# Performance work log

Hardware: AMD Instinct MI355X
Metric: run time of the kernel (lower is better)

Reference implementation:

```python
import jax, jax.numpy as jnp
import numpy as np

N = 100000
E = 1600000
D_IN = 128
D_OUT = 128
BN_EPS = 1e-5


def setup_inputs() -> dict:
    key = jax.random.key(0)
    k1, k2, k3, k4 = jax.random.split(key, 4)
    x = jax.random.normal(k1, (N, D_IN), dtype=jnp.float32)
    edge_index = jax.random.randint(k2, (2, E), 0, N, dtype=jnp.int64)
    # Linear params (torch: y = x @ W.T + b)
    lim = 1.0 / np.sqrt(D_IN)
    W = jax.random.uniform(k3, (D_OUT, D_IN), minval=-lim, maxval=lim, dtype=jnp.float32)
    b = jax.random.uniform(k4, (D_OUT,), minval=-lim, maxval=lim, dtype=jnp.float32)
    # BatchNorm1d affine params (torch defaults: weight=1, bias=0)
    gamma = jnp.ones((D_OUT,), dtype=jnp.float32)
    beta = jnp.zeros((D_OUT,), dtype=jnp.float32)
    return {"x": x, "edge_index": edge_index, "W": W, "b": b,
            "gamma": gamma, "beta": beta, "batch_size": 32}


def reference(x, edge_index, W, b, gamma, beta, batch_size):
    # Linear
    h = x @ W.T + b  # (N, D_OUT)
    num_nodes = h.shape[0]
    row, col = edge_index[0], edge_index[1]
    # Gather neighbor features and scatter-add into destination rows
    agg = jax.ops.segment_sum(h[col], row, num_segments=num_nodes)  # (N, D_OUT)
    cnt = jax.ops.segment_sum(jnp.ones((edge_index.shape[1], 1), dtype=h.dtype),
                              row, num_segments=num_nodes)  # (N, 1)
    agg = agg / (cnt + 1e-8)
    # Residual
    h = h + agg
    # BatchNorm1d, training mode (batch statistics, biased variance)
    mean = jnp.mean(h, axis=0)
    var = jnp.mean((h - mean) ** 2, axis=0)
    out = (h - mean) * jax.lax.rsqrt(var + BN_EPS) * gamma + beta
    return out
```

## Files before the change

kernel.cpp:

```cpp
#include <hip/hip_runtime.h>

#define BN_EPS_F 1e-5f
#define MAXB 128
#define BIN_CHUNK 4096
#define BIN_EPT 16

static __device__ __forceinline__ float bf2f(unsigned short u) {
  union { unsigned int i; float f; } c; c.i = ((unsigned int)u) << 16; return c.f;
}
static __device__ __forceinline__ unsigned short f2bf(float f) {
  union { float f; unsigned int i; } c; c.f = f;
  unsigned int r = c.i + 0x7FFFu + ((c.i >> 16) & 1u);
  return (unsigned short)(r >> 16);
}

__global__ void transpose_W_kernel(const float* __restrict__ W, float* __restrict__ Wt) {
  int idx = blockIdx.x * 256 + threadIdx.x;
  if (idx < 128 * 128) {
    int j = idx >> 7, k = idx & 127;
    Wt[(k << 7) + j] = W[idx];
  }
}

__global__ __launch_bounds__(256) void linear_kernel(
    const float* __restrict__ x, const float* __restrict__ Wt,
    const float* __restrict__ bias, unsigned short* __restrict__ h, int n_nodes) {
  __shared__ float xt[32 * 128];
  const int t = threadIdx.x;
  const int tile = blockIdx.x << 5;
  {
    const float4* xg = reinterpret_cast<const float4*>(x) + ((size_t)tile << 5);
    float4* xl = reinterpret_cast<float4*>(xt);
#pragma unroll
    for (int i = 0; i < 4; ++i) xl[t + i * 256] = xg[t + i * 256];
  }
  __syncthreads();
  const int jq = (t & 31) << 2;
  const int g = t >> 5;
  const float* xr0 = &xt[(g * 4 + 0) << 7];
  const float* xr1 = &xt[(g * 4 + 1) << 7];
  const float* xr2 = &xt[(g * 4 + 2) << 7];
  const float* xr3 = &xt[(g * 4 + 3) << 7];
  float4 a0 = {0, 0, 0, 0}, a1 = {0, 0, 0, 0}, a2 = {0, 0, 0, 0}, a3 = {0, 0, 0, 0};
#pragma unroll 8
  for (int k = 0; k < 128; ++k) {
    float4 w = *reinterpret_cast<const float4*>(&Wt[(k << 7) + jq]);
    float x0 = xr0[k], x1 = xr1[k], x2 = xr2[k], x3 = xr3[k];
    a0.x = fmaf(x0, w.x, a0.x); a0.y = fmaf(x0, w.y, a0.y);
    a0.z = fmaf(x0, w.z, a0.z); a0.w = fmaf(x0, w.w, a0.w);
    a1.x = fmaf(x1, w.x, a1.x); a1.y = fmaf(x1, w.y, a1.y);
    a1.z = fmaf(x1, w.z, a1.z); a1.w = fmaf(x1, w.w, a1.w);
    a2.x = fmaf(x2, w.x, a2.x); a2.y = fmaf(x2, w.y, a2.y);
    a2.z = fmaf(x2, w.z, a2.z); a2.w = fmaf(x2, w.w, a2.w);
    a3.x = fmaf(x3, w.x, a3.x); a3.y = fmaf(x3, w.y, a3.y);
    a3.z = fmaf(x3, w.z, a3.z); a3.w = fmaf(x3, w.w, a3.w);
  }
  float4 bb = *reinterpret_cast<const float4*>(&bias[jq]);
  a0.x += bb.x; a0.y += bb.y; a0.z += bb.z; a0.w += bb.w;
  a1.x += bb.x; a1.y += bb.y; a1.z += bb.z; a1.w += bb.w;
  a2.x += bb.x; a2.y += bb.y; a2.z += bb.z; a2.w += bb.w;
  a3.x += bb.x; a3.y += bb.y; a3.z += bb.z; a3.w += bb.w;
  const int nb = tile + (g << 2);
  ushort4 p0 = {f2bf(a0.x), f2bf(a0.y), f2bf(a0.z), f2bf(a0.w)};
  ushort4 p1 = {f2bf(a1.x), f2bf(a1.y), f2bf(a1.z), f2bf(a1.w)};
  ushort4 p2 = {f2bf(a2.x), f2bf(a2.y), f2bf(a2.z), f2bf(a2.w)};
  ushort4 p3 = {f2bf(a3.x), f2bf(a3.y), f2bf(a3.z), f2bf(a3.w)};
  *reinterpret_cast<ushort4*>(&h[((size_t)(nb + 0) << 7) + jq]) = p0;
  *reinterpret_cast<ushort4*>(&h[((size_t)(nb + 1) << 7) + jq]) = p1;
  *reinterpret_cast<ushort4*>(&h[((size_t)(nb + 2) << 7) + jq]) = p2;
  *reinterpret_cast<ushort4*>(&h[((size_t)(nb + 3) << 7) + jq]) = p3;
}

__global__ __launch_bounds__(256) void bucket_hist_kernel(
    const int* __restrict__ row, int* __restrict__ bhist, int e_total, int nb) {
  __shared__ int bh[MAXB];
  const int t = threadIdx.x;
  if (t < MAXB) bh[t] = 0;
  __syncthreads();
  int i = blockIdx.x * 256 + t;
  const int stride = gridDim.x * 256;
  for (; i < e_total; i += stride) atomicAdd(&bh[row[i] >> 10], 1);
  __syncthreads();
  if (t < nb) {
    int c = bh[t];
    if (c) atomicAdd(&bhist[t], c);
  }
}

__global__ void bucket_scan_kernel(const int* __restrict__ bhist, int* __restrict__ bbase,
                                   int* __restrict__ bcursor, int nb, int e_total) {
  __shared__ int sd[MAXB];
  const int t = threadIdx.x;
  int v = (t < nb) ? bhist[t] : 0;
  sd[t] = v;
  __syncthreads();
  for (int off = 1; off < MAXB; off <<= 1) {
    int u = (t >= off) ? sd[t - off] : 0;
    __syncthreads();
    sd[t] += u;
    __syncthreads();
  }
  int excl = sd[t] - v;
  if (t < nb) { bbase[t] = excl; bcursor[t] = excl; }
  if (t == 0) bbase[nb] = e_total;
}

__global__ __launch_bounds__(256) void bin_kernel(
    const int* __restrict__ row, const int* __restrict__ col,
    int* __restrict__ bcursor, unsigned int* __restrict__ pairs, int e_total, int nb) {
  __shared__ int scount[MAXB];
  __shared__ int gbase[MAXB];
  const int t = threadIdx.x;
  if (t < MAXB) scount[t] = 0;
  __syncthreads();
  const int base = blockIdx.x * BIN_CHUNK;
  int bkt[BIN_EPT], slot[BIN_EPT];
  unsigned int pk[BIN_EPT];
#pragma unroll
  for (int k = 0; k < BIN_EPT; ++k) {
    int i = base + t + (k << 8);
    bkt[k] = -1;
    if (i < e_total) {
      int r = row[i], c = col[i];
      bkt[k] = r >> 10;
      pk[k] = ((unsigned int)(r & 1023) << 17) | (unsigned int)c;
      slot[k] = atomicAdd(&scount[bkt[k]], 1);
    }
  }
  __syncthreads();
  if (t < nb) {
    int c = scount[t];
    gbase[t] = c ? atomicAdd(&bcursor[t], c) : 0;
  }
  __syncthreads();
#pragma unroll
  for (int k = 0; k < BIN_EPT; ++k) {
    if (bkt[k] >= 0) pairs[gbase[bkt[k]] + slot[k]] = pk[k];
  }
}

__global__ __launch_bounds__(256) void csr_kernel(
    const unsigned int* __restrict__ pairs, const int* __restrict__ bbase,
    int* __restrict__ rowptr, int* __restrict__ scol, int n, int e_total) {
  __shared__ int lh[1024];
  __shared__ int sscan[256];
  const int b = blockIdx.x;
  const int t = threadIdx.x;
  const int node_base = b << 10;
  const int nn = min(1024, n - node_base);
  const int p0 = bbase[b], p1 = bbase[b + 1];
  for (int j = t; j < 1024; j += 256) lh[j] = 0;
  __syncthreads();
  for (int i = p0 + t; i < p1; i += 256) {
    atomicAdd(&lh[pairs[i] >> 17], 1);
  }
  __syncthreads();
  const int v0 = lh[4 * t + 0], v1 = lh[4 * t + 1], v2 = lh[4 * t + 2], v3 = lh[4 * t + 3];
  const int s = v0 + v1 + v2 + v3;
  sscan[t] = s;
  __syncthreads();
  for (int off = 1; off < 256; off <<= 1) {
    int u = (t >= off) ? sscan[t - off] : 0;
    __syncthreads();
    sscan[t] += u;
    __syncthreads();
  }
  const int excl = sscan[t] - s;
  const int c0 = excl, c1 = excl + v0, c2 = c1 + v1, c3 = c2 + v2;
  if (4 * t + 0 < nn) rowptr[node_base + 4 * t + 0] = p0 + c0;
  if (4 * t + 1 < nn) rowptr[node_base + 4 * t + 1] = p0 + c1;
  if (4 * t + 2 < nn) rowptr[node_base + 4 * t + 2] = p0 + c2;
  if (4 * t + 3 < nn) rowptr[node_base + 4 * t + 3] = p0 + c3;
  __syncthreads();
  lh[4 * t + 0] = c0; lh[4 * t + 1] = c1; lh[4 * t + 2] = c2; lh[4 * t + 3] = c3;
  __syncthreads();
  for (int i = p0 + t; i < p1; i += 256) {
    unsigned int p = pairs[i];
    int pl = atomicAdd(&lh[p >> 17], 1);
    scol[p0 + pl] = (int)(p & 0x1FFFFu);
  }
  if (b == 0 && t == 0) rowptr[n] = e_total;
}

__global__ __launch_bounds__(256) void agg_kernel(
    const unsigned short* __restrict__ h, const int* __restrict__ rowptr,
    const int* __restrict__ scol, float* __restrict__ out,
    float* __restrict__ stat_sum, float* __restrict__ stat_sumsq, int n_nodes) {
  const int t = threadIdx.x;
  const int wave = t >> 6, lane = t & 63;
  const int f0 = lane << 1;
  float lsx = 0.f, lsy = 0.f, lqx = 0.f, lqy = 0.f;
  const int wstride = gridDim.x << 2;
  for (int node = (blockIdx.x << 2) + wave; node < n_nodes; node += wstride) {
    const int r0 = rowptr[node], r1 = rowptr[node + 1];
    ushort2 hv = *reinterpret_cast<const ushort2*>(&h[((size_t)node << 7) + f0]);
    float s0x = 0.f, s0y = 0.f, s1x = 0.f, s1y = 0.f;
    int e = r0;
    for (; e + 3 < r1; e += 4) {
      int c0 = scol[e], c1 = scol[e + 1], c2 = scol[e + 2], c3 = scol[e + 3];
      ushort2 v0 = *reinterpret_cast<const ushort2*>(&h[((size_t)c0 << 7) + f0]);
      ushort2 v1 = *reinterpret_cast<const ushort2*>(&h[((size_t)c1 << 7) + f0]);
      ushort2 v2 = *reinterpret_cast<const ushort2*>(&h[((size_t)c2 << 7) + f0]);
      ushort2 v3 = *reinterpret_cast<const ushort2*>(&h[((size_t)c3 << 7) + f0]);
      s0x += bf2f(v0.x); s0y += bf2f(v0.y);
      s1x += bf2f(v1.x); s1y += bf2f(v1.y);
      s0x += bf2f(v2.x); s0y += bf2f(v2.y);
      s1x += bf2f(v3.x); s1y += bf2f(v3.y);
    }
    for (; e < r1; ++e) {
      int c0 = scol[e];
      ushort2 v0 = *reinterpret_cast<const ushort2*>(&h[((size_t)c0 << 7) + f0]);
      s0x += bf2f(v0.x); s0y += bf2f(v0.y);
    }
    const float inv = 1.0f / ((float)(r1 - r0) + 1e-8f);
    const float vx = fmaf(s0x + s1x, inv, bf2f(hv.x));
    const float vy = fmaf(s0y + s1y, inv, bf2f(hv.y));
    float2 o; o.x = vx; o.y = vy;
    *reinterpret_cast<float2*>(&out[((size_t)node << 7) + f0]) = o;
    lsx += vx; lsy += vy;
    lqx = fmaf(vx, vx, lqx); lqy = fmaf(vy, vy, lqy);
  }
  __shared__ float reds[4][128];
  __shared__ float redq[4][128];
  reds[wave][f0] = lsx; reds[wave][f0 + 1] = lsy;
  redq[wave][f0] = lqx; redq[wave][f0 + 1] = lqy;
  __syncthreads();
  if (t < 128) {
    float s = reds[0][t] + reds[1][t] + reds[2][t] + reds[3][t];
    float q = redq[0][t] + redq[1][t] + redq[2][t] + redq[3][t];
    atomicAdd(&stat_sum[t], s);
    atomicAdd(&stat_sumsq[t], q);
  }
}

__global__ void finalize_kernel(const float* __restrict__ ssum, const float* __restrict__ ssq,
                                const float* __restrict__ gamma, const float* __restrict__ beta,
                                float* __restrict__ scale, float* __restrict__ shift, int n) {
  const int t = threadIdx.x;
  const float invn = 1.0f / (float)n;
  float mean = ssum[t] * invn;
  float var = ssq[t] * invn - mean * mean;
  float sc = gamma[t] * rsqrtf(var + BN_EPS_F);
  scale[t] = sc;
  shift[t] = beta[t] - mean * sc;
}

__global__ __launch_bounds__(256) void bn_kernel(float* __restrict__ out,
                                                 const float* __restrict__ scale,
                                                 const float* __restrict__ shift, int n_nodes) {
  __shared__ float sc[128], sh[128];
  if (threadIdx.x < 128) {
    sc[threadIdx.x] = scale[threadIdx.x];
    sh[threadIdx.x] = shift[threadIdx.x];
  }
  __syncthreads();
  const int total4 = n_nodes * 32;
  int i = blockIdx.x * 256 + threadIdx.x;
  const int stride = gridDim.x * 256;
  float4* o4 = reinterpret_cast<float4*>(out);
  for (; i < total4; i += stride) {
    float4 v = o4[i];
    const int fq = (i & 31) << 2;
    v.x = fmaf(v.x, sc[fq + 0], sh[fq + 0]);
    v.y = fmaf(v.y, sc[fq + 1], sh[fq + 1]);
    v.z = fmaf(v.z, sc[fq + 2], sh[fq + 2]);
    v.w = fmaf(v.w, sc[fq + 3], sh[fq + 3]);
    o4[i] = v;
  }
}

extern "C" void kernel_launch(void* const* d_in, const int* in_sizes, int n_in,
                              void* d_out, int out_size, void* d_ws, size_t ws_size,
                              hipStream_t stream) {
  const float* x     = (const float*)d_in[0];
  const int*   ei    = (const int*)d_in[1];
  const float* W     = (const float*)d_in[2];
  const float* bias  = (const float*)d_in[3];
  const float* gamma = (const float*)d_in[4];
  const float* beta  = (const float*)d_in[5];
  const int n = in_sizes[0] / 128;
  const int e = in_sizes[1] / 2;
  const int* row = ei;
  const int* col = ei + e;
  float* out = (float*)d_out;

  char* base = (char*)d_ws;
  size_t off = 0;
  auto carve = [&](size_t bytes) -> char* {
    char* p = base + off;
    off += (bytes + 255) & ~(size_t)255;
    return p;
  };
  unsigned short* h = (unsigned short*)carve((size_t)n * 128 * 2);
  float* Wt       = (float*)carve(128 * 128 * 4);
  unsigned int* pairs = (unsigned int*)carve((size_t)e * 4);
  int*   scol     = (int*)carve((size_t)e * 4);
  int*   rowptr   = (int*)carve((size_t)(n + 1) * 4);
  int*   bcursor  = (int*)carve(MAXB * 4);
  int*   bbase    = (int*)carve((MAXB + 1) * 4);
  float* scale    = (float*)carve(512);
  float* shift    = (float*)carve(512);
  char*  zbase    = base + off;
  int*   bhist    = (int*)carve(MAXB * 4);
  float* ssum     = (float*)carve(512);
  float* ssq      = (float*)carve(512);
  size_t zlen     = (size_t)((base + off) - zbase);
  (void)ws_size; (void)n_in; (void)out_size;

  const int nb = (n + 1023) >> 10;
  const int bin_grid = (e + BIN_CHUNK - 1) / BIN_CHUNK;

  hipMemsetAsync(zbase, 0, zlen, stream);
  transpose_W_kernel<<<64, 256, 0, stream>>>(W, Wt);
  linear_kernel<<<n / 32, 256, 0, stream>>>(x, Wt, bias, h, n);
  bucket_hist_kernel<<<256, 256, 0, stream>>>(row, bhist, e, nb);
  bucket_scan_kernel<<<1, MAXB, 0, stream>>>(bhist, bbase, bcursor, nb, e);
  bin_kernel<<<bin_grid, 256, 0, stream>>>(row, col, bcursor, pairs, e, nb);
  csr_kernel<<<nb, 256, 0, stream>>>(pairs, bbase, rowptr, scol, n, e);
  agg_kernel<<<3200, 256, 0, stream>>>(h, rowptr, scol, out, ssum, ssq, n);
  finalize_kernel<<<1, 128, 0, stream>>>(ssum, ssq, gamma, beta, scale, shift, n);
  bn_kernel<<<2048, 256, 0, stream>>>(out, scale, shift, n);
}
```

Measured before the change: 379.2 us.

## Use bf16 MFMA for linear layer and split edges across half-waves in aggregation

```diff
diff --git a/kernel.cpp b/kernel.cpp
--- a/kernel.cpp
+++ b/kernel.cpp
@@ -5,6 +5,9 @@
 #define BIN_CHUNK 4096
 #define BIN_EPT 16
 
+typedef __attribute__((ext_vector_type(8))) short bf16x8;
+typedef __attribute__((ext_vector_type(4))) float f32x4;
+
 static __device__ __forceinline__ float bf2f(unsigned short u) {
   union { unsigned int i; float f; } c; c.i = ((unsigned int)u) << 16; return c.f;
 }
@@ -14,61 +17,64 @@
   return (unsigned short)(r >> 16);
 }
 
-__global__ void transpose_W_kernel(const float* __restrict__ W, float* __restrict__ Wt) {
+__global__ void wfrag_kernel(const float* __restrict__ W, unsigned short* __restrict__ wfrag) {
   int idx = blockIdx.x * 256 + threadIdx.x;
-  if (idx < 128 * 128) {
-    int j = idx >> 7, k = idx & 127;
-    Wt[(k << 7) + j] = W[idx];
-  }
+  int e = idx & 7, l = (idx >> 3) & 63, kk = (idx >> 9) & 3, jt = idx >> 11;
+  int j = jt * 16 + (l & 15);
+  int k = kk * 32 + ((l >> 4) << 3) + e;
+  wfrag[idx] = f2bf(W[j * 128 + k]);
 }
 
 __global__ __launch_bounds__(256) void linear_kernel(
-    const float* __restrict__ x, const float* __restrict__ Wt,
-    const float* __restrict__ bias, unsigned short* __restrict__ h, int n_nodes) {
-  __shared__ float xt[32 * 128];
-  const int t = threadIdx.x;
-  const int tile = blockIdx.x << 5;
-  {
-    const float4* xg = reinterpret_cast<const float4*>(x) + ((size_t)tile << 5);
-    float4* xl = reinterpret_cast<float4*>(xt);
-#pragma unroll
-    for (int i = 0; i < 4; ++i) xl[t + i * 256] = xg[t + i * 256];
-  }
-  __syncthreads();
-  const int jq = (t & 31) << 2;
-  const int g = t >> 5;
-  const float* xr0 = &xt[(g * 4 + 0) << 7];
-  const float* xr1 = &xt[(g * 4 + 1) << 7];
-  const float* xr2 = &xt[(g * 4 + 2) << 7];
-  const float* xr3 = &xt[(g * 4 + 3) << 7];
-  float4 a0 = {0, 0, 0, 0}, a1 = {0, 0, 0, 0}, a2 = {0, 0, 0, 0}, a3 = {0, 0, 0, 0};
-#pragma unroll 8
-  for (int k = 0; k < 128; ++k) {
-    float4 w = *reinterpret_cast<const float4*>(&Wt[(k << 7) + jq]);
-    float x0 = xr0[k], x1 = xr1[k], x2 = xr2[k], x3 = xr3[k];
-    a0.x = fmaf(x0, w.x, a0.x); a0.y = fmaf(x0, w.y, a0.y);
-    a0.z = fmaf(x0, w.z, a0.z); a0.w = fmaf(x0, w.w, a0.w);
-    a1.x = fmaf(x1, w.x, a1.x); a1.y = fmaf(x1, w.y, a1.y);
-    a1.z = fmaf(x1, w.z, a1.z); a1.w = fmaf(x1, w.w, a1.w);
-    a2.x = fmaf(x2, w.x, a2.x); a2.y = fmaf(x2, w.y, a2.y);
-    a2.z = fmaf(x2, w.z, a2.z); a2.w = fmaf(x2, w.w, a2.w);
-    a3.x = fmaf(x3, w.x, a3.x); a3.y = fmaf(x3, w.y, a3.y);
-    a3.z = fmaf(x3, w.z, a3.z); a3.w = fmaf(x3, w.w, a3.w);
-  }
-  float4 bb = *reinterpret_cast<const float4*>(&bias[jq]);
-  a0.x += bb.x; a0.y += bb.y; a0.z += bb.z; a0.w += bb.w;
-  a1.x += bb.x; a1.y += bb.y; a1.z += bb.z; a1.w += bb.w;
-  a2.x += bb.x; a2.y += bb.y; a2.z += bb.z; a2.w += bb.w;
-  a3.x += bb.x; a3.y += bb.y; a3.z += bb.z; a3.w += bb.w;
-  const int nb = tile + (g << 2);
-  ushort4 p0 = {f2bf(a0.x), f2bf(a0.y), f2bf(a0.z), f2bf(a0.w)};
-  ushort4 p1 = {f2bf(a1.x), f2bf(a1.y), f2bf(a1.z), f2bf(a1.w)};
-  ushort4 p2 = {f2bf(a2.x), f2bf(a2.y), f2bf(a2.z), f2bf(a2.w)};
-  ushort4 p3 = {f2bf(a3.x), f2bf(a3.y), f2bf(a3.z), f2bf(a3.w)};
-  *reinterpret_cast<ushort4*>(&h[((size_t)(nb + 0) << 7) + jq]) = p0;
-  *reinterpret_cast<ushort4*>(&h[((size_t)(nb + 1) << 7) + jq]) = p1;
-  *reinterpret_cast<ushort4*>(&h[((size_t)(nb + 2) << 7) + jq]) = p2;
-  *reinterpret_cast<ushort4*>(&h[((size_t)(nb + 3) << 7) + jq]) = p3;
+    const float* __restrict__ x, const unsigned short* __restrict__ wfrag,
+    const float* __restrict__ bias, ushort4* __restrict__ h4, int n) {
+  __shared__ unsigned short els[4][16 * 128];
+  const int t = threadIdx.x;
+  const int w = t >> 6, lane = t & 63;
+  const int base = blockIdx.x * 64 + w * 16;
+  const int row = base + (lane & 15);
+  const int rowc = row < n ? row : (n - 1);
+  const float4* xr = reinterpret_cast<const float4*>(x) + (size_t)rowc * 32;
+  const bf16x8* bf = reinterpret_cast<const bf16x8*>(wfrag);
+
+  f32x4 acc[8];
+#pragma unroll
+  for (int jt = 0; jt < 8; ++jt) acc[jt] = (f32x4){0.f, 0.f, 0.f, 0.f};
+
+#pragma unroll
+  for (int kk = 0; kk < 4; ++kk) {
+    float4 lo = xr[kk * 8 + ((lane >> 4) << 1)];
+    float4 hi = xr[kk * 8 + ((lane >> 4) << 1) + 1];
+    bf16x8 a;
+    a[0] = (short)f2bf(lo.x); a[1] = (short)f2bf(lo.y);
+    a[2] = (short)f2bf(lo.z); a[3] = (short)f2bf(lo.w);
+    a[4] = (short)f2bf(hi.x); a[5] = (short)f2bf(hi.y);
+    a[6] = (short)f2bf(hi.z); a[7] = (short)f2bf(hi.w);
+#pragma unroll
+    for (int jt = 0; jt < 8; ++jt) {
+      bf16x8 b = bf[(jt * 4 + kk) * 64 + lane];
+      acc[jt] = __builtin_amdgcn_mfma_f32_16x16x32_bf16(a, b, acc[jt], 0, 0, 0);
+    }
+  }
+
+  unsigned short* ep = els[w];
+#pragma unroll
+  for (int jt = 0; jt < 8; ++jt) {
+    float bv = bias[jt * 16 + (lane & 15)];
+#pragma unroll
+    for (int r = 0; r < 4; ++r) {
+      int orow = ((lane >> 4) << 2) + r;
+      ep[orow * 128 + jt * 16 + (lane & 15)] = f2bf(acc[jt][r] + bv);
+    }
+  }
+  const ushort4* ep4 = reinterpret_cast<const ushort4*>(ep);
+#pragma unroll
+  for (int i = 0; i < 8; ++i) {
+    int idx = i * 64 + lane;
+    int r2 = idx >> 5, c4 = idx & 31;
+    int grow = base + r2;
+    if (grow < n) h4[(size_t)grow * 32 + c4] = ep4[idx];
+  }
 }
 
 __global__ __launch_bounds__(256) void bucket_hist_kernel(
@@ -183,53 +189,65 @@
 }
 
 __global__ __launch_bounds__(256) void agg_kernel(
-    const unsigned short* __restrict__ h, const int* __restrict__ rowptr,
+    const ushort4* __restrict__ h4, const int* __restrict__ rowptr,
     const int* __restrict__ scol, float* __restrict__ out,
     float* __restrict__ stat_sum, float* __restrict__ stat_sumsq, int n_nodes) {
   const int t = threadIdx.x;
   const int wave = t >> 6, lane = t & 63;
-  const int f0 = lane << 1;
-  float lsx = 0.f, lsy = 0.f, lqx = 0.f, lqy = 0.f;
+  const int half = lane >> 5, q = lane & 31;
+  float ls0 = 0.f, ls1 = 0.f, ls2 = 0.f, ls3 = 0.f;
+  float lq0 = 0.f, lq1 = 0.f, lq2 = 0.f, lq3 = 0.f;
   const int wstride = gridDim.x << 2;
   for (int node = (blockIdx.x << 2) + wave; node < n_nodes; node += wstride) {
     const int r0 = rowptr[node], r1 = rowptr[node + 1];
-    ushort2 hv = *reinterpret_cast<const ushort2*>(&h[((size_t)node << 7) + f0]);
-    float s0x = 0.f, s0y = 0.f, s1x = 0.f, s1y = 0.f;
-    int e = r0;
-    for (; e + 3 < r1; e += 4) {
-      int c0 = scol[e], c1 = scol[e + 1], c2 = scol[e + 2], c3 = scol[e + 3];
-      ushort2 v0 = *reinterpret_cast<const ushort2*>(&h[((size_t)c0 << 7) + f0]);
-      ushort2 v1 = *reinterpret_cast<const ushort2*>(&h[((size_t)c1 << 7) + f0]);
-      ushort2 v2 = *reinterpret_cast<const ushort2*>(&h[((size_t)c2 << 7) + f0]);
-      ushort2 v3 = *reinterpret_cast<const ushort2*>(&h[((size_t)c3 << 7) + f0]);
-      s0x += bf2f(v0.x); s0y += bf2f(v0.y);
-      s1x += bf2f(v1.x); s1y += bf2f(v1.y);
-      s0x += bf2f(v2.x); s0y += bf2f(v2.y);
-      s1x += bf2f(v3.x); s1y += bf2f(v3.y);
-    }
-    for (; e < r1; ++e) {
+    float a0 = 0.f, a1 = 0.f, a2 = 0.f, a3 = 0.f;
+    int e = r0 + half;
+    for (; e + 2 < r1; e += 4) {
+      int c0 = scol[e], c1 = scol[e + 2];
+      ushort4 v0 = h4[(size_t)c0 * 32 + q];
+      ushort4 v1 = h4[(size_t)c1 * 32 + q];
+      a0 += bf2f(v0.x) + bf2f(v1.x);
+      a1 += bf2f(v0.y) + bf2f(v1.y);
+      a2 += bf2f(v0.z) + bf2f(v1.z);
+      a3 += bf2f(v0.w) + bf2f(v1.w);
+    }
+    if (e < r1) {
       int c0 = scol[e];
-      ushort2 v0 = *reinterpret_cast<const ushort2*>(&h[((size_t)c0 << 7) + f0]);
-      s0x += bf2f(v0.x); s0y += bf2f(v0.y);
-    }
-    const float inv = 1.0f / ((float)(r1 - r0) + 1e-8f);
-    const float vx = fmaf(s0x + s1x, inv, bf2f(hv.x));
-    const float vy = fmaf(s0y + s1y, inv, bf2f(hv.y));
-    float2 o; o.x = vx; o.y = vy;
-    *reinterpret_cast<float2*>(&out[((size_t)node << 7) + f0]) = o;
-    lsx += vx; lsy += vy;
-    lqx = fmaf(vx, vx, lqx); lqy = fmaf(vy, vy, lqy);
+      ushort4 v0 = h4[(size_t)c0 * 32 + q];
+      a0 += bf2f(v0.x); a1 += bf2f(v0.y); a2 += bf2f(v0.z); a3 += bf2f(v0.w);
+    }
+    a0 += __shfl_xor(a0, 32, 64);
+    a1 += __shfl_xor(a1, 32, 64);
+    a2 += __shfl_xor(a2, 32, 64);
+    a3 += __shfl_xor(a3, 32, 64);
+    if (half == 0) {
+      ushort4 hv = h4[(size_t)node * 32 + q];
+      const float inv = 1.0f / ((float)(r1 - r0) + 1e-8f);
+      float v0 = fmaf(a0, inv, bf2f(hv.x));
+      float v1 = fmaf(a1, inv, bf2f(hv.y));
+      float v2 = fmaf(a2, inv, bf2f(hv.z));
+      float v3 = fmaf(a3, inv, bf2f(hv.w));
+      float4 o; o.x = v0; o.y = v1; o.z = v2; o.w = v3;
+      *reinterpret_cast<float4*>(&out[(size_t)node * 128 + q * 4]) = o;
+      ls0 += v0; ls1 += v1; ls2 += v2; ls3 += v3;
+      lq0 = fmaf(v0, v0, lq0); lq1 = fmaf(v1, v1, lq1);
+      lq2 = fmaf(v2, v2, lq2); lq3 = fmaf(v3, v3, lq3);
+    }
   }
   __shared__ float reds[4][128];
   __shared__ float redq[4][128];
-  reds[wave][f0] = lsx; reds[wave][f0 + 1] = lsy;
-  redq[wave][f0] = lqx; redq[wave][f0 + 1] = lqy;
+  if (half == 0) {
+    float4 s; s.x = ls0; s.y = ls1; s.z = ls2; s.w = ls3;
+    float4 qq; qq.x = lq0; qq.y = lq1; qq.z = lq2; qq.w = lq3;
+    *reinterpret_cast<float4*>(&reds[wave][q * 4]) = s;
+    *reinterpret_cast<float4*>(&redq[wave][q * 4]) = qq;
+  }
   __syncthreads();
   if (t < 128) {
     float s = reds[0][t] + reds[1][t] + reds[2][t] + reds[3][t];
-    float q = redq[0][t] + redq[1][t] + redq[2][t] + redq[3][t];
+    float qv = redq[0][t] + redq[1][t] + redq[2][t] + redq[3][t];
     atomicAdd(&stat_sum[t], s);
-    atomicAdd(&stat_sumsq[t], q);
+    atomicAdd(&stat_sumsq[t], qv);
   }
 }
 
@@ -292,7 +310,7 @@
     return p;
   };
   unsigned short* h = (unsigned short*)carve((size_t)n * 128 * 2);
-  float* Wt       = (float*)carve(128 * 128 * 4);
+  unsigned short* wfrag = (unsigned short*)carve(128 * 128 * 2);
   unsigned int* pairs = (unsigned int*)carve((size_t)e * 4);
   int*   scol     = (int*)carve((size_t)e * 4);
   int*   rowptr   = (int*)carve((size_t)(n + 1) * 4);
@@ -309,15 +327,16 @@
 
   const int nb = (n + 1023) >> 10;
   const int bin_grid = (e + BIN_CHUNK - 1) / BIN_CHUNK;
+  const int lin_grid = (n + 63) / 64;
 
   hipMemsetAsync(zbase, 0, zlen, stream);
-  transpose_W_kernel<<<64, 256, 0, stream>>>(W, Wt);
-  linear_kernel<<<n / 32, 256, 0, stream>>>(x, Wt, bias, h, n);
+  wfrag_kernel<<<64, 256, 0, stream>>>(W, wfrag);
+  linear_kernel<<<lin_grid, 256, 0, stream>>>(x, wfrag, bias, (ushort4*)h, n);
   bucket_hist_kernel<<<256, 256, 0, stream>>>(row, bhist, e, nb);
   bucket_scan_kernel<<<1, MAXB, 0, stream>>>(bhist, bbase, bcursor, nb, e);
   bin_kernel<<<bin_grid, 256, 0, stream>>>(row, col, bcursor, pairs, e, nb);
   csr_kernel<<<nb, 256, 0, stream>>>(pairs, bbase, rowptr, scol, n, e);
-  agg_kernel<<<3200, 256, 0, stream>>>(h, rowptr, scol, out, ssum, ssq, n);
+  agg_kernel<<<3200, 256, 0, stream>>>((const ushort4*)h, rowptr, scol, out, ssum, ssq, n);
   finalize_kernel<<<1, 128, 0, stream>>>(ssum, ssq, gamma, beta, scale, shift, n);
   bn_kernel<<<2048, 256, 0, stream>>>(out, scale, shift, n);
 }
```

Result: faster. 349.0 us (-8.0%).
